# Kernel tuning notes

Measured on AMD Instinct MI355X. Metric: run time of the kernel, lower is better.

## Reference

```python
import jax, jax.numpy as jnp
import numpy as np

NUM_HEADS = 16
HEAD_DIM = 64
D_DEC = 1024
D_ENC = 1024
R = 256  # kv_lora_rank
LN_EPS = 1e-5


def setup_inputs() -> dict:
    key = jax.random.key(0)
    ks = jax.random.split(key, 8)
    B, SQ, SK = 4, 2048, 4096
    query = jax.random.normal(ks[0], (B, SQ, D_DEC), dtype=jnp.float32)
    encoder_output = jax.random.normal(ks[1], (B, SK, D_ENC), dtype=jnp.float32)
    s = 0.02
    Wq = jax.random.normal(ks[2], (NUM_HEADS * HEAD_DIM, D_DEC), dtype=jnp.float32) * s
    Wkva = jax.random.normal(ks[3], (R, D_ENC), dtype=jnp.float32) * s
    ln_g = jnp.ones((R,), dtype=jnp.float32)
    ln_b = jnp.zeros((R,), dtype=jnp.float32)
    Wkvb = jax.random.normal(ks[4], (NUM_HEADS * 2 * HEAD_DIM, R), dtype=jnp.float32) * s
    Wout = jax.random.normal(ks[5], (D_DEC, NUM_HEADS * HEAD_DIM), dtype=jnp.float32) * s
    return {"query": query, "encoder_output": encoder_output, "Wq": Wq,
            "Wkva": Wkva, "ln_g": ln_g, "ln_b": ln_b, "Wkvb": Wkvb, "Wout": Wout}


def reference(query, encoder_output, Wq, Wkva, ln_g, ln_b, Wkvb, Wout):
    B, SQ, _ = query.shape
    SK = encoder_output.shape[1]
    H, Dh = NUM_HEADS, HEAD_DIM

    # q projection -> [B, H, SQ, Dh]
    q = jnp.einsum('bsd,ed->bse', query, Wq).reshape(B, SQ, H, Dh).transpose(0, 2, 1, 3)

    # low-rank KV compression + layernorm
    c = jnp.einsum('bsd,rd->bsr', encoder_output, Wkva)  # [B, SK, R]
    mu = jnp.mean(c, axis=-1, keepdims=True)
    var = jnp.mean(jnp.square(c - mu), axis=-1, keepdims=True)
    c = (c - mu) * jax.lax.rsqrt(var + LN_EPS) * ln_g + ln_b

    # decompress to K,V: [B, SK, H, 2*Dh] -> split
    kv = jnp.einsum('bsr,er->bse', c, Wkvb).reshape(B, SK, H, 2 * Dh).transpose(0, 2, 1, 3)
    k, v = kv[..., :Dh], kv[..., Dh:]

    scale = 1.0 / np.sqrt(Dh).astype(np.float32)
    scores = jnp.einsum('bhqd,bhkd->bhqk', q, k) * scale
    attn = jax.nn.softmax(scores, axis=-1)  # dropout is identity in eval / p=0
    o = jnp.einsum('bhqk,bhkd->bhqd', attn, v)
    o = o.transpose(0, 2, 1, 3).reshape(B, SQ, H * Dh)
    return jnp.einsum('bse,de->bsd', o, Wout)
```

## Files before the change

kernel.cpp:

```cpp
#include <hip/hip_runtime.h>

#define LOG2E 1.4426950408889634f

typedef __attribute__((ext_vector_type(8))) short short8;
typedef __attribute__((ext_vector_type(4))) float f32x4;
typedef __attribute__((ext_vector_type(16))) float f32x16;
typedef __attribute__((ext_vector_type(4))) unsigned u32x4;

__device__ inline unsigned short f2bf(float f) {
  unsigned u = __float_as_uint(f);
  u += 0x7fffu + ((u >> 16) & 1u);
  return (unsigned short)(u >> 16);
}

#define MFMA16(a, b, c) __builtin_amdgcn_mfma_f32_16x16x32_bf16((a), (b), (c), 0, 0, 0)
#define MFMA32(a, b, c) __builtin_amdgcn_mfma_f32_32x32x16_bf16((a), (b), (c), 0, 0, 0)

#define GLDS16(gp, lp)                                                              \
  __builtin_amdgcn_global_load_lds((const __attribute__((address_space(1))) void*)(gp), \
                                   (__attribute__((address_space(3))) void*)(lp), 16, 0, 0)

__device__ inline f32x4 zero4() {
  f32x4 z = {0.f, 0.f, 0.f, 0.f};
  return z;
}
__device__ inline f32x16 zero16() {
  f32x16 z = {0.f, 0.f, 0.f, 0.f, 0.f, 0.f, 0.f, 0.f, 0.f, 0.f, 0.f, 0.f, 0.f, 0.f, 0.f, 0.f};
  return z;
}
__device__ inline unsigned cvtpk_bf16(float a, float b) {
  unsigned r;
  asm("v_cvt_pk_bf16_f32 %0, %1, %2" : "=v"(r) : "v"(a), "v"(b));
  return r;
}
__device__ inline void plswap(unsigned& a, unsigned& b) {
  asm("v_permlane32_swap_b32 %0, %1" : "+v"(a), "+v"(b));
}

__global__ __launch_bounds__(256) void k_cast6(
    const float* __restrict__ e, const float* __restrict__ q, const float* __restrict__ wq,
    const float* __restrict__ wo, const float* __restrict__ wb, const float* __restrict__ wa,
    unsigned short* __restrict__ eo, unsigned short* __restrict__ qo, unsigned short* __restrict__ wqo,
    unsigned short* __restrict__ woo, unsigned short* __restrict__ wbo, unsigned short* __restrict__ wao) {
  int i = (blockIdx.x * 256 + threadIdx.x) * 4;
  const float* src;
  unsigned short* dst;
  int off;
  if (i < 16777216) { src = e; dst = eo; off = i; }
  else if (i < 25165824) { src = q; dst = qo; off = i - 16777216; }
  else if (i < 26214400) { src = wq; dst = wqo; off = i - 25165824; }
  else if (i < 27262976) { src = wo; dst = woo; off = i - 26214400; }
  else if (i < 27787264) { src = wb; dst = wbo; off = i - 27262976; }
  else { src = wa; dst = wao; off = i - 27787264; }
  float4 v = *(const float4*)(src + off);
  unsigned lo = (unsigned)f2bf(v.x) | ((unsigned)f2bf(v.y) << 16);
  unsigned hi = (unsigned)f2bf(v.z) | ((unsigned)f2bf(v.w) << 16);
  *(uint2*)(dst + off) = make_uint2(lo, hi);
}

__global__ __launch_bounds__(256, 2) void k_qproj(const unsigned short* __restrict__ A,
                                                  const unsigned short* __restrict__ Bw,
                                                  unsigned short* __restrict__ Qout) {
  __shared__ __align__(16) short As[128 * 32];
  __shared__ __align__(16) short Bs[128 * 32];
  const int K = 1024;
  int tid = threadIdx.x;
  int w = tid >> 6, lane = tid & 63, quad = lane >> 4, c = lane & 15;
  int m0 = blockIdx.x * 128, n0 = blockIdx.y * 128;
  int wm = (w >> 1) * 64, wn = (w & 1) * 64;
  f32x4 acc[4][4];
#pragma unroll
  for (int i = 0; i < 4; i++)
#pragma unroll
    for (int j = 0; j < 4; j++) acc[i][j] = zero4();

  for (int k0 = 0; k0 < K; k0 += 32) {
#pragma unroll
    for (int i = 0; i < 2; i++) {
      int seg = w * 2 + i;
      int bo = seg * 1024 + lane * 16;
      int row = bo >> 6, col = (bo & 63) >> 1;
      GLDS16(A + (size_t)(m0 + row) * K + k0 + col, (char*)As + seg * 1024);
      GLDS16(Bw + (size_t)(n0 + row) * K + k0 + col, (char*)Bs + seg * 1024);
    }
    __syncthreads();
    short8 af[4], bfr[4];
#pragma unroll
    for (int i = 0; i < 4; i++) {
      af[i] = *(const short8*)&As[(wm + i * 16 + c) * 32 + quad * 8];
      bfr[i] = *(const short8*)&Bs[(wn + i * 16 + c) * 32 + quad * 8];
    }
#pragma unroll
    for (int mi = 0; mi < 4; mi++)
#pragma unroll
      for (int ni = 0; ni < 4; ni++) acc[mi][ni] = MFMA16(af[mi], bfr[ni], acc[mi][ni]);
    __syncthreads();
  }
  const float scale = 0.125f * LOG2E;
#pragma unroll
  for (int mi = 0; mi < 4; mi++) {
    int rowb = m0 + wm + mi * 16 + quad * 4;
#pragma unroll
    for (int ni = 0; ni < 4; ni++) {
      int col = n0 + wn + ni * 16 + c;
      int h = col >> 6, d = col & 63;
#pragma unroll
      for (int r = 0; r < 4; r++) {
        int row = rowb + r;
        int b = row >> 11, sq = row & 2047;
        Qout[(((size_t)(b * 16 + h)) * 2048 + sq) * 64 + d] = f2bf(acc[mi][ni][r] * scale);
      }
    }
  }
}

__global__ __launch_bounds__(256, 2) void k_cln(const unsigned short* __restrict__ E,
                                                const unsigned short* __restrict__ Wa,
                                                const float* __restrict__ g, const float* __restrict__ bb,
                                                unsigned short* __restrict__ Cout) {
  __shared__ __align__(16) short As[64 * 32];
  __shared__ __align__(16) short Bs[256 * 32];
  __shared__ float redS[4][64], redQ[4][64];
  __shared__ float gS[256], bS[256];
  const int K = 1024;
  int tid = threadIdx.x;
  int w = tid >> 6, lane = tid & 63, quad = lane >> 4, c = lane & 15;
  int m0 = blockIdx.x * 64;
  gS[tid] = g[tid];
  bS[tid] = bb[tid];
  f32x4 acc[4][4];
#pragma unroll
  for (int i = 0; i < 4; i++)
#pragma unroll
    for (int j = 0; j < 4; j++) acc[i][j] = zero4();

  for (int k0 = 0; k0 < K; k0 += 32) {
    {
      int bo = w * 1024 + lane * 16;
      int row = bo >> 6, col = (bo & 63) >> 1;
      GLDS16(E + (size_t)(m0 + row) * K + k0 + col, (char*)As + w * 1024);
    }
#pragma unroll
    for (int i = 0; i < 4; i++) {
      int seg = w * 4 + i;
      int bo = seg * 1024 + lane * 16;
      int row = bo >> 6, col = (bo & 63) >> 1;
      GLDS16(Wa + (size_t)row * K + k0 + col, (char*)Bs + seg * 1024);
    }
    __syncthreads();
    short8 af[4], bfr[4];
#pragma unroll
    for (int i = 0; i < 4; i++) {
      af[i] = *(const short8*)&As[(i * 16 + c) * 32 + quad * 8];
      bfr[i] = *(const short8*)&Bs[(w * 64 + i * 16 + c) * 32 + quad * 8];
    }
#pragma unroll
    for (int mi = 0; mi < 4; mi++)
#pragma unroll
      for (int ni = 0; ni < 4; ni++) acc[mi][ni] = MFMA16(af[mi], bfr[ni], acc[mi][ni]);
    __syncthreads();
  }
  float ps[4][4], pq[4][4];
#pragma unroll
  for (int mi = 0; mi < 4; mi++)
#pragma unroll
    for (int r = 0; r < 4; r++) {
      float s = 0.f, q = 0.f;
#pragma unroll
      for (int ni = 0; ni < 4; ni++) {
        float x = acc[mi][ni][r];
        s += x;
        q += x * x;
      }
      for (int m = 1; m < 16; m <<= 1) {
        s += __shfl_xor(s, m, 64);
        q += __shfl_xor(q, m, 64);
      }
      ps[mi][r] = s;
      pq[mi][r] = q;
    }
  if (c == 0) {
#pragma unroll
    for (int mi = 0; mi < 4; mi++)
#pragma unroll
      for (int r = 0; r < 4; r++) {
        int row = mi * 16 + quad * 4 + r;
        redS[w][row] = ps[mi][r];
        redQ[w][row] = pq[mi][r];
      }
  }
  __syncthreads();
  float muv[4][4], rsv[4][4];
#pragma unroll
  for (int mi = 0; mi < 4; mi++)
#pragma unroll
    for (int r = 0; r < 4; r++) {
      int row = mi * 16 + quad * 4 + r;
      float S = redS[0][row] + redS[1][row] + redS[2][row] + redS[3][row];
      float Q = redQ[0][row] + redQ[1][row] + redQ[2][row] + redQ[3][row];
      float mu = S * (1.f / 256.f);
      float var = Q * (1.f / 256.f) - mu * mu;
      muv[mi][r] = mu;
      rsv[mi][r] = rsqrtf(var + 1e-5f);
    }
#pragma unroll
  for (int mi = 0; mi < 4; mi++)
#pragma unroll
    for (int ni = 0; ni < 4; ni++) {
      int col = w * 64 + ni * 16 + c;
#pragma unroll
      for (int r = 0; r < 4; r++) {
        int row = m0 + mi * 16 + quad * 4 + r;
        float y = (acc[mi][ni][r] - muv[mi][r]) * rsv[mi][r] * gS[col] + bS[col];
        Cout[(size_t)row * 256 + col] = f2bf(y);
      }
    }
}

__global__ __launch_bounds__(256, 2) void k_kv(const unsigned short* __restrict__ A,
                                               const unsigned short* __restrict__ Bw,
                                               unsigned short* __restrict__ Kb,
                                               unsigned short* __restrict__ Vb) {
  __shared__ __align__(16) short As[128 * 32];
  __shared__ __align__(16) short Bs[128 * 32];
  const int K = 256;
  int tid = threadIdx.x;
  int w = tid >> 6, lane = tid & 63, quad = lane >> 4, c = lane & 15;
  int m0 = blockIdx.x * 128, n0 = blockIdx.y * 128;
  int wm = (w >> 1) * 64, wn = (w & 1) * 64;
  f32x4 acc[4][4];
#pragma unroll
  for (int i = 0; i < 4; i++)
#pragma unroll
    for (int j = 0; j < 4; j++) acc[i][j] = zero4();

  for (int k0 = 0; k0 < K; k0 += 32) {
#pragma unroll
    for (int i = 0; i < 2; i++) {
      int seg = w * 2 + i;
      int bo = seg * 1024 + lane * 16;
      int row = bo >> 6, col = (bo & 63) >> 1;
      GLDS16(A + (size_t)(m0 + row) * K + k0 + col, (char*)As + seg * 1024);
      GLDS16(Bw + (size_t)(n0 + row) * K + k0 + col, (char*)Bs + seg * 1024);
    }
    __syncthreads();
    short8 af[4], bfr[4];
#pragma unroll
    for (int i = 0; i < 4; i++) {
      af[i] = *(const short8*)&As[(wm + i * 16 + c) * 32 + quad * 8];
      bfr[i] = *(const short8*)&Bs[(wn + i * 16 + c) * 32 + quad * 8];
    }
#pragma unroll
    for (int mi = 0; mi < 4; mi++)
#pragma unroll
      for (int ni = 0; ni < 4; ni++) acc[mi][ni] = MFMA16(af[mi], bfr[ni], acc[mi][ni]);
    __syncthreads();
  }
#pragma unroll
  for (int mi = 0; mi < 4; mi++) {
    int rowb = m0 + wm + mi * 16 + quad * 4;
#pragma unroll
    for (int ni = 0; ni < 4; ni++) {
      int col = n0 + wn + ni * 16 + c;
      int h = col >> 7, rr = col & 127;
#pragma unroll
      for (int r = 0; r < 4; r++) {
        int row = rowb + r;
        int b = row >> 12, sk = row & 4095;
        int kt = sk >> 6, ki = sk & 63;
        size_t base = ((size_t)(b * 16 + h)) * 262144 + (size_t)kt * 4096;
        float x = acc[mi][ni][r];
        if (rr < 64) {
          int d = rr;
          int half = ki >> 5, l31k = ki & 31, ds = d >> 4, dhi = (d >> 3) & 1, j = d & 7;
          Kb[base + (size_t)((half * 4 + ds) * 64 + l31k + 32 * dhi) * 8 + j] = f2bf(x);
        } else {
          int d = rr - 64;
          int dt = d >> 5, sg = ki >> 4, khi = (ki >> 3) & 1, j = ki & 7;
          Vb[base + (size_t)((dt * 4 + sg) * 64 + (d & 31) + 32 * khi) * 8 + j] = f2bf(x);
        }
      }
    }
  }
}

__global__ __launch_bounds__(128, 2) void k_attn(const unsigned short* __restrict__ Qb,
                                                 const unsigned short* __restrict__ Kb,
                                                 const unsigned short* __restrict__ Vb,
                                                 unsigned short* __restrict__ Ob) {
  __shared__ __align__(16) short KVs[16384];
  int tid = threadIdx.x;
  int w = tid >> 6, lane = tid & 63;
  int l31 = lane & 31, hi = lane >> 5;
  int qt = blockIdx.x, bh = blockIdx.y;

  const char* Kg = (const char*)Kb + (size_t)bh * 524288;
  const char* Vg = (const char*)Vb + (size_t)bh * 524288;
  const char* sgbase = (w ? Vg : Kg) + lane * 16;

  const unsigned short* Qrow = Qb + ((size_t)bh * 2048 + qt * 128 + w * 64 + l31) * 64 + hi * 8;
  short8 qf[2][4];
#pragma unroll
  for (int qb = 0; qb < 2; qb++)
#pragma unroll
    for (int ds = 0; ds < 4; ds++) qf[qb][ds] = *(const short8*)(Qrow + qb * 2048 + ds * 16);

  f32x16 O[2][2];
  float lp[2] = {0.f, 0.f};
#pragma unroll
  for (int i = 0; i < 2; i++)
#pragma unroll
    for (int j = 0; j < 2; j++) O[i][j] = zero16();

#pragma unroll
  for (int i = 0; i < 8; i++) GLDS16(sgbase + i * 1024, (char*)KVs + w * 8192 + i * 1024);
#pragma unroll
  for (int i = 0; i < 8; i++) GLDS16(sgbase + 8192 + i * 1024, (char*)KVs + 16384 + w * 8192 + i * 1024);
  sgbase += 16384;

  for (int kt = 0; kt < 64; kt++) {
    if (kt == 63)
      asm volatile("s_waitcnt vmcnt(0)\n\ts_barrier" ::: "memory");
    else
      asm volatile("s_waitcnt vmcnt(8)\n\ts_barrier" ::: "memory");

    const char* Kl = (const char*)KVs + (kt & 1) * 16384 + lane * 16;
    const char* Vl = Kl + 8192;

#pragma unroll
    for (int h = 0; h < 2; h++) {
      short8 kf[4];
#pragma unroll
      for (int ds = 0; ds < 4; ds++) kf[ds] = *(const short8*)(Kl + (h * 4 + ds) * 1024);
      short8 paf[2][2];
#pragma unroll
      for (int qb = 0; qb < 2; qb++) {
        f32x16 S = zero16();
#pragma unroll
        for (int ds = 0; ds < 4; ds++) S = MFMA32(kf[ds], qf[qb][ds], S);
        float pp[8];
        unsigned u[8];
#pragma unroll
        for (int m = 0; m < 8; m++) {
          float p0 = __builtin_amdgcn_exp2f(S[2 * m]);
          float p1 = __builtin_amdgcn_exp2f(S[2 * m + 1]);
          pp[m] = p0 + p1;
          u[m] = cvtpk_bf16(p0, p1);
        }
        lp[qb] += ((pp[0] + pp[1]) + (pp[2] + pp[3])) + ((pp[4] + pp[5]) + (pp[6] + pp[7]));
        plswap(u[0], u[2]);
        plswap(u[1], u[3]);
        plswap(u[4], u[6]);
        plswap(u[5], u[7]);
        u32x4 w0 = {u[0], u[1], u[2], u[3]};
        u32x4 w1 = {u[4], u[5], u[6], u[7]};
        paf[qb][0] = __builtin_bit_cast(short8, w0);
        paf[qb][1] = __builtin_bit_cast(short8, w1);
      }
#pragma unroll
      for (int dt = 0; dt < 2; dt++)
#pragma unroll
        for (int s2 = 0; s2 < 2; s2++) {
          short8 vf = *(const short8*)(Vl + (dt * 4 + h * 2 + s2) * 1024);
#pragma unroll
          for (int qb = 0; qb < 2; qb++) O[qb][dt] = MFMA32(paf[qb][s2], vf, O[qb][dt]);
        }
    }
    asm volatile("s_barrier" ::: "memory");
    if (kt < 62) {
#pragma unroll
      for (int i = 0; i < 8; i++)
        GLDS16(sgbase + i * 1024, (char*)KVs + (kt & 1) * 16384 + w * 8192 + i * 1024);
      sgbase += 8192;
    }
  }

#pragma unroll
  for (int qb = 0; qb < 2; qb++) lp[qb] += __shfl_xor(lp[qb], 32, 64);
  int b = bh >> 4, hh = bh & 15;
#pragma unroll
  for (int qb = 0; qb < 2; qb++) {
#pragma unroll
    for (int r = 0; r < 16; r++) {
      int qrow = (r & 3) + 8 * (r >> 2) + 4 * hi;
      float inv = __builtin_amdgcn_rcpf(__shfl(lp[qb], qrow, 64));
      size_t orow = ((size_t)b * 2048 + qt * 128 + w * 64 + qb * 32 + qrow) * 1024 + hh * 64 + l31;
      Ob[orow] = f2bf(O[qb][0][r] * inv);
      Ob[orow + 32] = f2bf(O[qb][1][r] * inv);
    }
  }
}

__global__ __launch_bounds__(256, 2) void k_out(const unsigned short* __restrict__ A,
                                                const unsigned short* __restrict__ Bw,
                                                float* __restrict__ Out) {
  __shared__ __align__(16) short As[128 * 32];
  __shared__ __align__(16) short Bs[128 * 32];
  const int K = 1024;
  int tid = threadIdx.x;
  int w = tid >> 6, lane = tid & 63, quad = lane >> 4, c = lane & 15;
  int m0 = blockIdx.x * 128, n0 = blockIdx.y * 128;
  int wm = (w >> 1) * 64, wn = (w & 1) * 64;
  f32x4 acc[4][4];
#pragma unroll
  for (int i = 0; i < 4; i++)
#pragma unroll
    for (int j = 0; j < 4; j++) acc[i][j] = zero4();

  for (int k0 = 0; k0 < K; k0 += 32) {
#pragma unroll
    for (int i = 0; i < 2; i++) {
      int seg = w * 2 + i;
      int bo = seg * 1024 + lane * 16;
      int row = bo >> 6, col = (bo & 63) >> 1;
      GLDS16(A + (size_t)(m0 + row) * K + k0 + col, (char*)As + seg * 1024);
      GLDS16(Bw + (size_t)(n0 + row) * K + k0 + col, (char*)Bs + seg * 1024);
    }
    __syncthreads();
    short8 af[4], bfr[4];
#pragma unroll
    for (int i = 0; i < 4; i++) {
      af[i] = *(const short8*)&As[(wm + i * 16 + c) * 32 + quad * 8];
      bfr[i] = *(const short8*)&Bs[(wn + i * 16 + c) * 32 + quad * 8];
    }
#pragma unroll
    for (int mi = 0; mi < 4; mi++)
#pragma unroll
      for (int ni = 0; ni < 4; ni++) acc[mi][ni] = MFMA16(af[mi], bfr[ni], acc[mi][ni]);
    __syncthreads();
  }
#pragma unroll
  for (int mi = 0; mi < 4; mi++) {
    int rowb = m0 + wm + mi * 16 + quad * 4;
#pragma unroll
    for (int ni = 0; ni < 4; ni++) {
      int col = n0 + wn + ni * 16 + c;
#pragma unroll
      for (int r = 0; r < 4; r++) Out[(size_t)(rowb + r) * 1024 + col] = acc[mi][ni][r];
    }
  }
}

extern "C" void kernel_launch(void* const* d_in, const int* in_sizes, int n_in,
                              void* d_out, int out_size, void* d_ws, size_t ws_size,
                              hipStream_t stream) {
  const float* query = (const float*)d_in[0];
  const float* enc = (const float*)d_in[1];
  const float* Wq = (const float*)d_in[2];
  const float* Wkva = (const float*)d_in[3];
  const float* ln_g = (const float*)d_in[4];
  const float* ln_b = (const float*)d_in[5];
  const float* Wkvb = (const float*)d_in[6];
  const float* Wout = (const float*)d_in[7];
  if (ws_size < 81264640) return;

  char* ws = (char*)d_ws;
  unsigned short* wq_bf = (unsigned short*)(ws + 0);
  unsigned short* wa_bf = (unsigned short*)(ws + 2097152);
  unsigned short* wb_bf = (unsigned short*)(ws + 2621440);
  unsigned short* wo_bf = (unsigned short*)(ws + 3670016);
  unsigned short* qproj = (unsigned short*)(ws + 5767168);
  unsigned short* cln = (unsigned short*)(ws + 22544384);
  unsigned short* ebf_v = (unsigned short*)(ws + 30932992);
  unsigned short* qin_o = (unsigned short*)(ws + 64487424);
  unsigned short* kbuf = (unsigned short*)d_out;

  k_cast6<<<27392, 256, 0, stream>>>(enc, query, Wq, Wout, Wkvb, Wkva,
                                     ebf_v, qin_o, wq_bf, wo_bf, wb_bf, wa_bf);

  k_qproj<<<dim3(64, 8), 256, 0, stream>>>(qin_o, wq_bf, qproj);
  k_cln<<<256, 256, 0, stream>>>(ebf_v, wa_bf, ln_g, ln_b, cln);
  k_kv<<<dim3(128, 16), 256, 0, stream>>>(cln, wb_bf, kbuf, ebf_v);
  k_attn<<<dim3(16, 64), 128, 0, stream>>>(qproj, kbuf, ebf_v, qin_o);
  k_out<<<dim3(64, 8), 256, 0, stream>>>(qin_o, wo_bf, (float*)d_out);
}
```

Before: 403.8 us.

## Split attention tile across four waves with 32 query rows each

Result: slower. 417.0 us (+3.3%).

```diff
diff --git a/kernel.cpp b/kernel.cpp
--- a/kernel.cpp
+++ b/kernel.cpp
@@ -284,7 +284,7 @@
   }
 }
 
-__global__ __launch_bounds__(128, 2) void k_attn(const unsigned short* __restrict__ Qb,
+__global__ __launch_bounds__(256, 4) void k_attn(const unsigned short* __restrict__ Qb,
                                                  const unsigned short* __restrict__ Kb,
                                                  const unsigned short* __restrict__ Vb,
                                                  unsigned short* __restrict__ Ob) {
@@ -296,33 +296,28 @@
 
   const char* Kg = (const char*)Kb + (size_t)bh * 524288;
   const char* Vg = (const char*)Vb + (size_t)bh * 524288;
-  const char* sgbase = (w ? Vg : Kg) + lane * 16;
-
-  const unsigned short* Qrow = Qb + ((size_t)bh * 2048 + qt * 128 + w * 64 + l31) * 64 + hi * 8;
-  short8 qf[2][4];
-#pragma unroll
-  for (int qb = 0; qb < 2; qb++)
-#pragma unroll
-    for (int ds = 0; ds < 4; ds++) qf[qb][ds] = *(const short8*)(Qrow + qb * 2048 + ds * 16);
-
-  f32x16 O[2][2];
-  float lp[2] = {0.f, 0.f};
-#pragma unroll
-  for (int i = 0; i < 2; i++)
-#pragma unroll
-    for (int j = 0; j < 2; j++) O[i][j] = zero16();
-
-#pragma unroll
-  for (int i = 0; i < 8; i++) GLDS16(sgbase + i * 1024, (char*)KVs + w * 8192 + i * 1024);
-#pragma unroll
-  for (int i = 0; i < 8; i++) GLDS16(sgbase + 8192 + i * 1024, (char*)KVs + 16384 + w * 8192 + i * 1024);
+  int ldsseg = (w < 2) ? w * 4 : 8 + (w - 2) * 4;
+  const char* sgbase = ((w < 2) ? Kg + (w * 4) * 1024 : Vg + ((w - 2) * 4) * 1024) + lane * 16;
+
+  const unsigned short* Qrow = Qb + ((size_t)bh * 2048 + qt * 128 + w * 32 + l31) * 64 + hi * 8;
+  short8 qf[4];
+#pragma unroll
+  for (int ds = 0; ds < 4; ds++) qf[ds] = *(const short8*)(Qrow + ds * 16);
+
+  f32x16 O[2];
+  float lp = 0.f;
+#pragma unroll
+  for (int j = 0; j < 2; j++) O[j] = zero16();
+
+#pragma unroll
+  for (int i = 0; i < 4; i++) GLDS16(sgbase + i * 1024, (char*)KVs + (ldsseg + i) * 1024);
+#pragma unroll
+  for (int i = 0; i < 4; i++)
+    GLDS16(sgbase + 8192 + i * 1024, (char*)KVs + 16384 + (ldsseg + i) * 1024);
   sgbase += 16384;
 
   for (int kt = 0; kt < 64; kt++) {
-    if (kt == 63)
-      asm volatile("s_waitcnt vmcnt(0)\n\ts_barrier" ::: "memory");
-    else
-      asm volatile("s_waitcnt vmcnt(8)\n\ts_barrier" ::: "memory");
+    __syncthreads();
 
     const char* Kl = (const char*)KVs + (kt & 1) * 16384 + lane * 16;
     const char* Vl = Kl + 8192;
@@ -332,62 +327,53 @@
       short8 kf[4];
 #pragma unroll
       for (int ds = 0; ds < 4; ds++) kf[ds] = *(const short8*)(Kl + (h * 4 + ds) * 1024);
-      short8 paf[2][2];
-#pragma unroll
-      for (int qb = 0; qb < 2; qb++) {
-        f32x16 S = zero16();
-#pragma unroll
-        for (int ds = 0; ds < 4; ds++) S = MFMA32(kf[ds], qf[qb][ds], S);
-        float pp[8];
-        unsigned u[8];
-#pragma unroll
-        for (int m = 0; m < 8; m++) {
-          float p0 = __builtin_amdgcn_exp2f(S[2 * m]);
-          float p1 = __builtin_amdgcn_exp2f(S[2 * m + 1]);
-          pp[m] = p0 + p1;
-          u[m] = cvtpk_bf16(p0, p1);
-        }
-        lp[qb] += ((pp[0] + pp[1]) + (pp[2] + pp[3])) + ((pp[4] + pp[5]) + (pp[6] + pp[7]));
-        plswap(u[0], u[2]);
-        plswap(u[1], u[3]);
-        plswap(u[4], u[6]);
-        plswap(u[5], u[7]);
-        u32x4 w0 = {u[0], u[1], u[2], u[3]};
-        u32x4 w1 = {u[4], u[5], u[6], u[7]};
-        paf[qb][0] = __builtin_bit_cast(short8, w0);
-        paf[qb][1] = __builtin_bit_cast(short8, w1);
-      }
-#pragma unroll
-      for (int dt = 0; dt < 2; dt++)
-#pragma unroll
-        for (int s2 = 0; s2 < 2; s2++) {
-          short8 vf = *(const short8*)(Vl + (dt * 4 + h * 2 + s2) * 1024);
-#pragma unroll
-          for (int qb = 0; qb < 2; qb++) O[qb][dt] = MFMA32(paf[qb][s2], vf, O[qb][dt]);
-        }
-    }
-    asm volatile("s_barrier" ::: "memory");
+      f32x16 S = zero16();
+#pragma unroll
+      for (int ds = 0; ds < 4; ds++) S = MFMA32(kf[ds], qf[ds], S);
+      float lpa = 0.f, lpb = 0.f;
+      unsigned u[8];
+#pragma unroll
+      for (int m = 0; m < 8; m++) {
+        float p0 = __builtin_amdgcn_exp2f(S[2 * m]);
+        float p1 = __builtin_amdgcn_exp2f(S[2 * m + 1]);
+        if (m & 1) lpb += p0 + p1; else lpa += p0 + p1;
+        u[m] = cvtpk_bf16(p0, p1);
+      }
+      lp += lpa + lpb;
+      plswap(u[0], u[2]);
+      plswap(u[1], u[3]);
+      plswap(u[4], u[6]);
+      plswap(u[5], u[7]);
+      u32x4 w0 = {u[0], u[1], u[2], u[3]};
+      u32x4 w1 = {u[4], u[5], u[6], u[7]};
+      short8 paf0 = __builtin_bit_cast(short8, w0);
+      short8 paf1 = __builtin_bit_cast(short8, w1);
+#pragma unroll
+      for (int dt = 0; dt < 2; dt++) {
+        short8 vf0 = *(const short8*)(Vl + (dt * 4 + h * 2 + 0) * 1024);
+        short8 vf1 = *(const short8*)(Vl + (dt * 4 + h * 2 + 1) * 1024);
+        O[dt] = MFMA32(paf0, vf0, O[dt]);
+        O[dt] = MFMA32(paf1, vf1, O[dt]);
+      }
+    }
+    __syncthreads();
     if (kt < 62) {
 #pragma unroll
-      for (int i = 0; i < 8; i++)
-        GLDS16(sgbase + i * 1024, (char*)KVs + (kt & 1) * 16384 + w * 8192 + i * 1024);
+      for (int i = 0; i < 4; i++)
+        GLDS16(sgbase + i * 1024, (char*)KVs + (kt & 1) * 16384 + (ldsseg + i) * 1024);
       sgbase += 8192;
     }
   }
 
-#pragma unroll
-  for (int qb = 0; qb < 2; qb++) lp[qb] += __shfl_xor(lp[qb], 32, 64);
+  lp += __shfl_xor(lp, 32, 64);
   int b = bh >> 4, hh = bh & 15;
 #pragma unroll
-  for (int qb = 0; qb < 2; qb++) {
-#pragma unroll
-    for (int r = 0; r < 16; r++) {
-      int qrow = (r & 3) + 8 * (r >> 2) + 4 * hi;
-      float inv = __builtin_amdgcn_rcpf(__shfl(lp[qb], qrow, 64));
-      size_t orow = ((size_t)b * 2048 + qt * 128 + w * 64 + qb * 32 + qrow) * 1024 + hh * 64 + l31;
-      Ob[orow] = f2bf(O[qb][0][r] * inv);
-      Ob[orow + 32] = f2bf(O[qb][1][r] * inv);
-    }
+  for (int r = 0; r < 16; r++) {
+    int qrow = (r & 3) + 8 * (r >> 2) + 4 * hi;
+    float inv = __builtin_amdgcn_rcpf(__shfl(lp, qrow, 64));
+    size_t orow = ((size_t)b * 2048 + qt * 128 + w * 32 + qrow) * 1024 + hh * 64 + l31;
+    Ob[orow] = f2bf(O[0][r] * inv);
+    Ob[orow + 32] = f2bf(O[1][r] * inv);
   }
 }
 
@@ -471,6 +457,6 @@
   k_qproj<<<dim3(64, 8), 256, 0, stream>>>(qin_o, wq_bf, qproj);
   k_cln<<<256, 256, 0, stream>>>(ebf_v, wa_bf, ln_g, ln_b, cln);
   k_kv<<<dim3(128, 16), 256, 0, stream>>>(cln, wb_bf, kbuf, ebf_v);
-  k_attn<<<dim3(16, 64), 128, 0, stream>>>(qproj, kbuf, ebf_v, qin_o);
+  k_attn<<<dim3(16, 64), 256, 0, stream>>>(qproj, kbuf, ebf_v, qin_o);
   k_out<<<dim3(64, 8), 256, 0, stream>>>(qin_o, wo_bf, (float*)d_out);
 }
```
